# Kernel optimization log

Hardware: AMD Instinct MI355X
Metric: run time of the kernel (lower is better)

## Reference

```python
import jax, jax.numpy as jnp
import numpy as np

B, H, W, DIM = 2, 256, 256, 256
PDIM, HEADS = 128, 8
CH = PDIM // HEADS  # per-head channel dim (16)


def _dwconv3x3(x, w):
    # x: [b, c, h, w], w: [c, 1, 3, 3], depthwise (groups=c)
    return jax.lax.conv_general_dilated(
        x, w, window_strides=(1, 1), padding=((1, 1), (1, 1)),
        dimension_numbers=("NCHW", "OIHW", "NCHW"),
        feature_group_count=w.shape[0])


def setup_inputs() -> dict:
    key = jax.random.key(0)
    ks = jax.random.split(key, 8)

    def nrm(k, shape, fan):
        return jax.random.normal(k, shape, jnp.float32) / np.float32(np.sqrt(fan))

    x = jax.random.normal(ks[0], (B, H, W, DIM), jnp.float32)
    qkv_w = nrm(ks[1], (3 * PDIM, PDIM), PDIM)            # 1x1 conv, no bias
    dw_w = nrm(ks[2], (3 * PDIM, 1, 3, 3), 9)             # depthwise 3x3, no bias
    proj_w = nrm(ks[3], (DIM, DIM), DIM)                  # 1x1 conv, no bias
    g1_w = nrm(ks[4], (DIM // 2, DIM), DIM)               # gate conv1 (bias=True default)
    g1_b = jnp.zeros((DIM // 2,), jnp.float32)
    g2_w = nrm(ks[5], (1, DIM // 2), DIM // 2)            # gate conv2
    g2_b = jnp.zeros((1,), jnp.float32)
    temperature = jnp.ones((HEADS, 1, 1), jnp.float32)
    attn1 = jnp.array([0.2], jnp.float32)
    attn2 = jnp.array([0.2], jnp.float32)
    attn3 = jnp.array([0.2], jnp.float32)
    attn4 = jnp.array([0.2], jnp.float32)
    return dict(x=x, qkv_w=qkv_w, dw_w=dw_w, proj_w=proj_w, g1_w=g1_w,
                g1_b=g1_b, g2_w=g2_w, g2_b=g2_b, temperature=temperature,
                attn1=attn1, attn2=attn2, attn3=attn3, attn4=attn4)


def reference(x, qkv_w, dw_w, proj_w, g1_w, g1_b, g2_w, g2_b,
              temperature, attn1, attn2, attn3, attn4):
    xc = jnp.transpose(x, (0, 3, 1, 2))  # [b, dim, h, w]
    b, c, h, w = xc.shape
    x1, x2 = xc[:, :PDIM], xc[:, PDIM:]

    qkv = jnp.einsum('oc,bchw->bohw', qkv_w, x1)
    qkv = _dwconv3x3(qkv, dw_w)
    q, k, v = jnp.split(qkv, 3, axis=1)

    def to_heads(t):
        return t.reshape(b, HEADS, CH, h * w)  # [b, head, C, hw]

    q, k, v = to_heads(q), to_heads(k), to_heads(v)
    q = q / jnp.maximum(jnp.linalg.norm(q, axis=-1, keepdims=True), 1e-12)
    k = k / jnp.maximum(jnp.linalg.norm(k, axis=-1, keepdims=True), 1e-12)

    # gate -> scalar dynamic_k = int(C * mean(sigmoid(...)))
    g = jax.nn.relu(jnp.einsum('oc,bchw->bohw', g1_w, xc) + g1_b[None, :, None, None])
    g = jax.nn.sigmoid(jnp.einsum('oc,bchw->bohw', g2_w, g) + g2_b[None, :, None, None])
    dyn_k = jax.lax.stop_gradient(jnp.floor(CH * jnp.mean(g)))  # scalar float, grad-stopped like int()

    attn = jnp.einsum('bhcn,bhdn->bhcd', q, k) * temperature  # [b, head, C, C]
    # top-k mask via rank: rank[i,j] = position of attn[i,j] in descending sort of row i
    ranks = jnp.argsort(jnp.argsort(-attn, axis=-1), axis=-1)
    attn = jnp.where(ranks < dyn_k, attn, -jnp.inf)
    attn = jax.nn.softmax(attn, axis=-1)

    out_av = jnp.einsum('bhcd,bhdn->bhcn', attn, v)
    # out1..out4 are identical in the original; weighted sum collapses
    out = out_av * attn1 + out_av * attn2 + out_av * attn3 + out_av * attn4
    out = out.reshape(b, PDIM, h, w)
    out = jnp.einsum('oc,bchw->bohw', proj_w, jnp.concatenate([out, x2], axis=1))
    return jnp.transpose(out, (0, 2, 3, 1))  # [b, h, w, dim]
```

## Files before the change

kernel.cpp:

```cpp
#include <hip/hip_runtime.h>
#include <cstdint>
#include <cstddef>

typedef __attribute__((ext_vector_type(4))) float v4f;
typedef __attribute__((ext_vector_type(8))) short v8s;
typedef __attribute__((ext_vector_type(4))) short v4s;

__device__ __forceinline__ short f2bf(float f) {
  unsigned u = __float_as_uint(f);
  u += 0x7FFFu + ((u >> 16) & 1u);
  return (short)(u >> 16);
}
__device__ __forceinline__ float bf2f(short h) {
  return __uint_as_float(((unsigned)(unsigned short)h) << 16);
}
__device__ __forceinline__ v4f mfma16(v8s a, v8s b, v4f c) {
  return __builtin_amdgcn_mfma_f32_16x16x32_bf16(a, b, c, 0, 0, 0);
}

#define OFF_GRAM   0u
#define OFF_QN     32768u
#define OFF_KN     34816u
#define OFF_GSUM   36864u
#define OFF_ATTN   40960u
#define OFF_WQH    65536u
#define OFF_WQL    163840u
#define OFF_G1H    262144u
#define OFF_G1L    327680u
#define OFF_W2     393216u
#define OFF_QK     1048576u
#define OFF_V      135266304u
#define OFF_VOUT   168820736u

__global__ void k0_split(const float* __restrict__ qkv_w, const float* __restrict__ g1_w,
                         short* __restrict__ wqh, short* __restrict__ wql,
                         short* __restrict__ g1h, short* __restrict__ g1l) {
  const int t = blockIdx.x * 256 + threadIdx.x;
  if (t < 6144) {
    const int l = t & 63, ks = (t >> 6) & 3, g = t >> 8;
    const int n = g * 16 + (l & 15), k = ks * 32 + (l >> 4) * 8;
    v8s hi, lo;
#pragma unroll
    for (int j = 0; j < 8; ++j) {
      const float f = qkv_w[n * 128 + k + j];
      const short h = f2bf(f);
      hi[j] = h; lo[j] = f2bf(f - bf2f(h));
    }
    *(v8s*)(wqh + (size_t)t * 8) = hi;
    *(v8s*)(wql + (size_t)t * 8) = lo;
  } else if (t < 10240) {
    const int t2 = t - 6144;
    const int l = t2 & 63, ks2 = (t2 >> 6) & 7, g2 = t2 >> 9;
    const int n = g2 * 16 + (l & 15), k = ks2 * 32 + (l >> 4) * 8;
    v8s hi, lo;
#pragma unroll
    for (int j = 0; j < 8; ++j) {
      const float f = g1_w[n * 256 + k + j];
      const short h = f2bf(f);
      hi[j] = h; lo[j] = f2bf(f - bf2f(h));
    }
    *(v8s*)(g1h + (size_t)t2 * 8) = hi;
    *(v8s*)(g1l + (size_t)t2 * 8) = lo;
  }
}

__global__ __launch_bounds__(512, 4) void k1_qkv(const float* __restrict__ x,
                                                 const short* __restrict__ wqh,
                                                 const short* __restrict__ wql,
                                                 float* __restrict__ qkf,
                                                 short* __restrict__ vb) {
  __shared__ __align__(16) unsigned char sm[49152];
  const int tid = threadIdx.x;
  const size_t m0 = (size_t)blockIdx.x * 64;
  const int lane = tid & 63, wid = tid >> 6;
  const int wm = wid >> 2, wn = wid & 3;

  v8s pbh[3], pbl[3];
#pragma unroll
  for (int s = 0; s < 3; ++s) {
    const size_t off = ((size_t)((0 * 4 + wn) * 4 + s) * 64 + lane) * 8;
    pbh[s] = *(const v8s*)(wqh + off);
    pbl[s] = *(const v8s*)(wql + off);
  }

  {
    const int row = tid >> 3, c0 = (tid & 7) * 16;
    const float* src = x + (m0 + (size_t)row) * 256 + c0;
#pragma unroll
    for (int half = 0; half < 2; ++half) {
      v4f f0 = *(const v4f*)(src + half * 8);
      v4f f1 = *(const v4f*)(src + half * 8 + 4);
      v8s hi, lo;
#pragma unroll
      for (int j = 0; j < 4; ++j) {
        short h0 = f2bf(f0[j]); hi[j] = h0;   lo[j]   = f2bf(f0[j] - bf2f(h0));
        short h1 = f2bf(f1[j]); hi[4+j] = h1; lo[4+j] = f2bf(f1[j] - bf2f(h1));
      }
      const int col = c0 + half * 8;
      const int byo = (row * 256 + col * 2) ^ ((row & 7) << 4);
      *(v8s*)(sm + byo) = hi;
      *(v8s*)(sm + 16384 + byo) = lo;
    }
  }
  __syncthreads();
  v8s ah[4][2];
#pragma unroll
  for (int ks = 0; ks < 4; ++ks)
#pragma unroll
    for (int mi = 0; mi < 2; ++mi) {
      const int kb2 = (ks * 32 + ((lane >> 4) * 8)) * 2;
      const int m = wm * 32 + mi * 16 + (lane & 15);
      const int byoA = (m * 256 + kb2) ^ ((m & 7) << 4);
      ah[ks][mi] = *(const v8s*)(sm + byoA);
    }
  const v4f vz = {0.f, 0.f, 0.f, 0.f};
  v4f acc[6][2];
#pragma unroll
  for (int i = 0; i < 6; ++i) { acc[i][0] = vz; acc[i][1] = vz; }

#pragma unroll
  for (int s = 0; s < 24; ++s) {
    const int nc = s >> 2, ks = s & 3, slot = s % 3;
    const v8s bh = pbh[slot];
    const v8s bl = pbl[slot];
    if (s + 3 < 24) {
      const int s3 = s + 3, nc3 = s3 >> 2, ks3 = s3 & 3;
      const size_t off = ((size_t)((nc3 * 4 + wn) * 4 + ks3) * 64 + lane) * 8;
      pbh[slot] = *(const v8s*)(wqh + off);
      if (nc3 < 4) pbl[slot] = *(const v8s*)(wql + off);
    }
#pragma unroll
    for (int mi = 0; mi < 2; ++mi) {
      const int kb2 = (ks * 32 + ((lane >> 4) * 8)) * 2;
      const int m = wm * 32 + mi * 16 + (lane & 15);
      const int byoA = (m * 256 + kb2) ^ ((m & 7) << 4);
      acc[nc][mi] = mfma16(ah[ks][mi], bh, acc[nc][mi]);
      if (nc < 4) {
        const v8s alv = *(const v8s*)(sm + 16384 + byoA);
        acc[nc][mi] = mfma16(alv, bh, acc[nc][mi]);
        acc[nc][mi] = mfma16(ah[ks][mi], bl, acc[nc][mi]);
      }
    }
  }
#pragma unroll
  for (int nc = 0; nc < 4; ++nc)
#pragma unroll
    for (int mi = 0; mi < 2; ++mi)
#pragma unroll
      for (int r = 0; r < 4; ++r) {
        const int m = wm * 32 + mi * 16 + ((lane >> 4) * 4) + r;
        const int n = nc * 64 + wn * 16 + (lane & 15);
        qkf[(m0 + m) * 256 + n] = acc[nc][mi][r];
      }
  short* vtr = (short*)(sm + 32768);
#pragma unroll
  for (int nc = 4; nc < 6; ++nc)
#pragma unroll
    for (int mi = 0; mi < 2; ++mi)
#pragma unroll
      for (int r = 0; r < 4; ++r) {
        const int m = wm * 32 + mi * 16 + ((lane >> 4) * 4) + r;
        const int n = (nc - 4) * 64 + wn * 16 + (lane & 15);
        vtr[m * 128 + n] = f2bf(acc[nc][mi][r]);
      }
  __syncthreads();
  {
    const int base = tid * 8;
#pragma unroll
    for (int p = 0; p < 2; ++p) {
      const int flat = p * 4096 + base;
      const int row = flat >> 7, col = flat & 127;
      const v8s t = *(const v8s*)(vtr + row * 128 + col);
      *(v8s*)(vb + (m0 + row) * 128 + col) = t;
    }
  }
}

__global__ __launch_bounds__(512, 4) void k1_g(const float* __restrict__ x,
                                               const short* __restrict__ g1h,
                                               const short* __restrict__ g1l,
                                               const float* __restrict__ g1_b,
                                               const float* __restrict__ g2_w,
                                               const float* __restrict__ g2_b,
                                               double* __restrict__ gsum) {
  __shared__ __align__(16) unsigned char sm[32768];
  const int tid = threadIdx.x;
  const size_t m0 = (size_t)blockIdx.x * 64;
  const int lane = tid & 63, wid = tid >> 6;
  const int wm = wid >> 2, wn = wid & 3;
  const v4f vz = {0.f, 0.f, 0.f, 0.f};
  v4f acc[2][2];
  acc[0][0] = vz; acc[0][1] = vz; acc[1][0] = vz; acc[1][1] = vz;
  v8s pbh[3], pbl[3];
#pragma unroll
  for (int kc = 0; kc < 2; ++kc) {
#pragma unroll
    for (int s = 0; s < 3; ++s) {
      const int nc = s >> 2, ks = s & 3;
      const size_t off = ((size_t)((nc * 4 + wn) * 8 + kc * 4 + ks) * 64 + lane) * 8;
      pbh[s] = *(const v8s*)(g1h + off);
      pbl[s] = *(const v8s*)(g1l + off);
    }
    __syncthreads();
    {
      const int row = tid >> 3, c0 = (tid & 7) * 16;
      const float* src = x + (m0 + (size_t)row) * 256 + kc * 128 + c0;
#pragma unroll
      for (int half = 0; half < 2; ++half) {
        v4f f0 = *(const v4f*)(src + half * 8);
        v4f f1 = *(const v4f*)(src + half * 8 + 4);
        v8s hi, lo;
#pragma unroll
        for (int j = 0; j < 4; ++j) {
          short h0 = f2bf(f0[j]); hi[j] = h0;   lo[j]   = f2bf(f0[j] - bf2f(h0));
          short h1 = f2bf(f1[j]); hi[4+j] = h1; lo[4+j] = f2bf(f1[j] - bf2f(h1));
        }
        const int col = c0 + half * 8;
        const int byo = (row * 256 + col * 2) ^ ((row & 7) << 4);
        *(v8s*)(sm + byo) = hi;
        *(v8s*)(sm + 16384 + byo) = lo;
      }
    }
    __syncthreads();
    v8s ah[4][2];
#pragma unroll
    for (int ks = 0; ks < 4; ++ks)
#pragma unroll
      for (int mi = 0; mi < 2; ++mi) {
        const int kb2 = (ks * 32 + ((lane >> 4) * 8)) * 2;
        const int m = wm * 32 + mi * 16 + (lane & 15);
        const int byoA = (m * 256 + kb2) ^ ((m & 7) << 4);
        ah[ks][mi] = *(const v8s*)(sm + byoA);
      }
#pragma unroll
    for (int s = 0; s < 8; ++s) {
      const int nc = s >> 2, ks = s & 3, slot = s % 3;
      const v8s bh = pbh[slot];
      const v8s bl = pbl[slot];
      if (s + 3 < 8) {
        const int s3 = s + 3, nc3 = s3 >> 2, ks3 = s3 & 3;
        const size_t off = ((size_t)((nc3 * 4 + wn) * 8 + kc * 4 + ks3) * 64 + lane) * 8;
        pbh[slot] = *(const v8s*)(g1h + off);
        pbl[slot] = *(const v8s*)(g1l + off);
      }
#pragma unroll
      for (int mi = 0; mi < 2; ++mi) {
        const int kb2 = (ks * 32 + ((lane >> 4) * 8)) * 2;
        const int m = wm * 32 + mi * 16 + (lane & 15);
        const int byoA = (m * 256 + kb2) ^ ((m & 7) << 4);
        const v8s alv = *(const v8s*)(sm + 16384 + byoA);
        acc[nc][mi] = mfma16(ah[ks][mi], bh, acc[nc][mi]);
        acc[nc][mi] = mfma16(alv, bh, acc[nc][mi]);
        acc[nc][mi] = mfma16(ah[ks][mi], bl, acc[nc][mi]);
        acc[nc][mi] = mfma16(alv, bl, acc[nc][mi]);
      }
    }
  }
  __syncthreads();
  float* g2ws = (float*)sm;
  float* ldsg = (float*)(sm + 512);
  if (tid < 128) g2ws[tid] = g2_w[tid];
  if (tid < 64) ldsg[tid] = 0.f;
  __syncthreads();
  float bias[2], g2v[2];
#pragma unroll
  for (int nc = 0; nc < 2; ++nc) {
    const int n = nc * 64 + wn * 16 + (lane & 15);
    bias[nc] = g1_b[n];
    g2v[nc] = g2ws[n];
  }
#pragma unroll
  for (int mi = 0; mi < 2; ++mi)
#pragma unroll
    for (int r = 0; r < 4; ++r) {
      float part = 0.f;
#pragma unroll
      for (int nc = 0; nc < 2; ++nc) {
        float val = acc[nc][mi][r] + bias[nc];
        val = fmaxf(val, 0.f);
        part += val * g2v[nc];
      }
      part += __shfl_xor(part, 1, 16);
      part += __shfl_xor(part, 2, 16);
      part += __shfl_xor(part, 4, 16);
      part += __shfl_xor(part, 8, 16);
      if ((lane & 15) == 0)
        atomicAdd(&ldsg[wm * 32 + mi * 16 + ((lane >> 4) * 4) + r], part);
    }
  __syncthreads();
  if (tid < 64) {
    float pre = ldsg[tid] + g2_b[0];
    float g = 1.f / (1.f + expf(-pre));
#pragma unroll
    for (int mk = 1; mk < 64; mk <<= 1) g += __shfl_xor(g, mk, 64);
    if (tid == 0) atomicAdd(gsum, (double)g);
  }
}

__global__ __launch_bounds__(256, 4) void k2_conv(const float* __restrict__ qkf,
                                                  const short* __restrict__ vb,
                                                  const float* __restrict__ dw_w,
                                                  double* __restrict__ gram,
                                                  double* __restrict__ qn,
                                                  double* __restrict__ kn,
                                                  short* __restrict__ vbuf) {
  __shared__ __align__(16) unsigned char SM[25984];
  float* haloT = (float*)SM;
  short* vtr   = (short*)SM;
  float* wsm   = (float*)(SM + 20800);
  float* redQ  = (float*)(SM + 21376);
  float* redK  = (float*)(SM + 21632);
  float* gramW = (float*)(SM + 21888);

  const int tid = threadIdx.x;
  const int tile = blockIdx.x, h = blockIdx.y, b = blockIdx.z;
  const int px0 = (tile & 15) * 16, py0 = (tile >> 4) * 16;
  const int c = tid & 15, r = tid >> 4;
  const int lane = tid & 63, w4 = tid >> 6;

  auto stage = [&](int sec) {
    const int chbase = sec * 128 + h * 16;
#pragma unroll
    for (int i = 0; i < 6; ++i) {
      const int idx = tid + i * 256;
      if (idx < 1296) {
        const int p = idx >> 2, e4 = (idx & 3) * 4;
        const int row = p / 18, col = p - row * 18;
        const int gy = py0 - 1 + row, gx = px0 - 1 + col;
        v4f val = {0.f, 0.f, 0.f, 0.f};
        if (gy >= 0 && gy < 256 && gx >= 0 && gx < 256) {
          const size_t pix = (size_t)(b * 65536 + gy * 256 + gx);
          if (sec < 2) {
            val = *(const v4f*)(qkf + pix * 256 + sec * 128 + h * 16 + e4);
          } else {
            const v4s sv = *(const v4s*)(vb + pix * 128 + h * 16 + e4);
            val[0] = bf2f(sv[0]); val[1] = bf2f(sv[1]);
            val[2] = bf2f(sv[2]); val[3] = bf2f(sv[3]);
          }
        }
        haloT[(e4 + 0) * 325 + p] = val[0];
        haloT[(e4 + 1) * 325 + p] = val[1];
        haloT[(e4 + 2) * 325 + p] = val[2];
        haloT[(e4 + 3) * 325 + p] = val[3];
      }
    }
    if (tid < 144) wsm[tid] = dw_w[chbase * 9 + tid];
  };

  auto conv16 = [&](float* o) {
#pragma unroll
    for (int j = 0; j < 16; ++j) o[j] = 0.f;
#pragma unroll
    for (int dy = 0; dy < 3; ++dy) {
      const float* rp = haloT + c * 325 + (r + dy) * 18;
      float rowb[18];
#pragma unroll
      for (int xx = 0; xx < 18; ++xx) rowb[xx] = rp[xx];
      const float w0 = wsm[c * 9 + dy * 3 + 0];
      const float w1 = wsm[c * 9 + dy * 3 + 1];
      const float w2 = wsm[c * 9 + dy * 3 + 2];
#pragma unroll
      for (int j = 0; j < 16; ++j)
        o[j] += w0 * rowb[j] + w1 * rowb[j + 1] + w2 * rowb[j + 2];
    }
  };

  float qreg[16], kreg[16];

  stage(0);
  __syncthreads();
  conv16(qreg);
  {
    float s = 0.f;
#pragma unroll
    for (int j = 0; j < 16; ++j) s += qreg[j] * qreg[j];
    s += __shfl_xor(s, 16, 64);
    s += __shfl_xor(s, 32, 64);
    if (lane < 16) redQ[w4 * 16 + lane] = s;
  }
  __syncthreads();
  stage(1);
  __syncthreads();
  conv16(kreg);
  {
    float s = 0.f;
#pragma unroll
    for (int j = 0; j < 16; ++j) s += kreg[j] * kreg[j];
    s += __shfl_xor(s, 16, 64);
    s += __shfl_xor(s, 32, 64);
    if (lane < 16) redK[w4 * 16 + lane] = s;
  }
  {
    v4f acc = {0.f, 0.f, 0.f, 0.f};
    const int qt = lane >> 4;
    const bool hiHalf = (qt & 1);
#pragma unroll
    for (int f = 0; f < 2; ++f) {
      const int src = ((f * 2 + (qt >> 1)) << 4) | (lane & 15);
      v8s qh, ql, kh, kl;
#pragma unroll
      for (int j = 0; j < 8; ++j) {
        const float qa = __shfl(qreg[j], src, 64);
        const float qb = __shfl(qreg[j + 8], src, 64);
        const float ka = __shfl(kreg[j], src, 64);
        const float kb = __shfl(kreg[j + 8], src, 64);
        const float qv = hiHalf ? qb : qa;
        const float kv = hiHalf ? kb : ka;
        const short h1 = f2bf(qv); qh[j] = h1; ql[j] = f2bf(qv - bf2f(h1));
        const short h2 = f2bf(kv); kh[j] = h2; kl[j] = f2bf(kv - bf2f(h2));
      }
      acc = mfma16(qh, kh, acc);
      acc = mfma16(ql, kh, acc);
      acc = mfma16(qh, kl, acc);
      acc = mfma16(ql, kl, acc);
    }
#pragma unroll
    for (int rr = 0; rr < 4; ++rr)
      gramW[w4 * 256 + (qt * 4 + rr) * 16 + (lane & 15)] = acc[rr];
  }
  __syncthreads();
  stage(2);
  __syncthreads();
  float vv[16];
  conv16(vv);
  if (tid < 16) {
    const float t = redQ[tid] + redQ[16 + tid] + redQ[32 + tid] + redQ[48 + tid];
    atomicAdd(&qn[b * 128 + h * 16 + tid], (double)t);
  } else if (tid < 32) {
    const int cc = tid - 16;
    const float t = redK[cc] + redK[16 + cc] + redK[32 + cc] + redK[48 + cc];
    atomicAdd(&kn[b * 128 + h * 16 + cc], (double)t);
  }
  {
    const float g = gramW[tid] + gramW[256 + tid] + gramW[512 + tid] + gramW[768 + tid];
    atomicAdd(&gram[(size_t)(b * 8 + h) * 256 + tid], (double)g);
  }
  __syncthreads();
  {
#pragma unroll
    for (int j = 0; j < 16; ++j) vtr[(r * 16 + j) * 24 + c] = f2bf(vv[j]);
  }
  __syncthreads();
  {
    const v8s o0 = *(const v8s*)(vtr + tid * 24);
    const v8s o1 = *(const v8s*)(vtr + tid * 24 + 8);
    short* dst = vbuf + ((size_t)b * 65536 + (size_t)(py0 + (tid >> 4)) * 256 + (px0 + (tid & 15))) * 128 + h * 16;
    *(v8s*)dst = o0;
    *(v8s*)(dst + 8) = o1;
  }
}

__global__ void k3a_attn(const double* __restrict__ gram, const double* __restrict__ qn,
                         const double* __restrict__ kn, const double* __restrict__ gsum,
                         const float* __restrict__ temp,
                         const float* __restrict__ a1p, const float* __restrict__ a2p,
                         const float* __restrict__ a3p, const float* __restrict__ a4p,
                         float* __restrict__ attnw) {
  const int t = threadIdx.x;
  const int b = t >> 7, rem = t & 127, h = rem >> 4, c = rem & 15;
  const float qnv = fmaxf(sqrtf((float)qn[b * 128 + h * 16 + c]), 1e-12f);
  const float tv = temp[h];
  float a[16];
#pragma unroll
  for (int d = 0; d < 16; ++d) {
    const float knv = fmaxf(sqrtf((float)kn[b * 128 + h * 16 + d]), 1e-12f);
    a[d] = (float)gram[(size_t)(b * 8 + h) * 256 + c * 16 + d] / (qnv * knv) * tv;
  }
  const float dynk = floorf(16.f * (float)(gsum[0] / 131072.0));
  float mx = -INFINITY;
  bool keep[16];
#pragma unroll
  for (int d = 0; d < 16; ++d) {
    int rank = 0;
#pragma unroll
    for (int e = 0; e < 16; ++e)
      rank += ((a[e] > a[d]) || ((a[e] == a[d]) && (e < d))) ? 1 : 0;
    keep[d] = ((float)rank < dynk);
    if (keep[d]) mx = fmaxf(mx, a[d]);
  }
  float ssum = 0.f, wvv[16];
#pragma unroll
  for (int d = 0; d < 16; ++d) {
    wvv[d] = keep[d] ? expf(a[d] - mx) : 0.f;
    ssum += wvv[d];
  }
  const float satt = a1p[0] + a2p[0] + a3p[0] + a4p[0];
  const float sc = satt / ssum;
#pragma unroll
  for (int d = 0; d < 16; ++d) attnw[t * 16 + d] = wvv[d] * sc;
}

__global__ void k3b_fold(const float* __restrict__ proj_w, const float* __restrict__ attnw,
                         short* __restrict__ W2f) {
  const int g = blockIdx.x, b = blockIdx.y;
  const int ks = threadIdx.x >> 6, lane = threadIdx.x & 63;
  const int o = g * 16 + (lane & 15);
  const int k0 = ks * 32 + (lane >> 4) * 8;
  v8s outv;
  if (k0 < 128) {
    const int h = k0 >> 4, d0 = k0 & 15;
    float s[8];
#pragma unroll
    for (int j = 0; j < 8; ++j) s[j] = 0.f;
#pragma unroll
    for (int i = 0; i < 16; ++i) {
      const float pw = proj_w[o * 256 + h * 16 + i];
#pragma unroll
      for (int j = 0; j < 8; ++j)
        s[j] += pw * attnw[((b * 8 + h) * 16 + i) * 16 + d0 + j];
    }
#pragma unroll
    for (int j = 0; j < 8; ++j) outv[j] = f2bf(s[j]);
  } else {
#pragma unroll
    for (int j = 0; j < 8; ++j) outv[j] = f2bf(proj_w[o * 256 + k0 + j]);
  }
  *(v8s*)(W2f + ((size_t)(b * 128 + g * 8 + ks) * 64 + lane) * 8) = outv;
}

__global__ __launch_bounds__(512, 4) void k4_out(const short* __restrict__ vbuf,
                                                 const float* __restrict__ x,
                                                 const short* __restrict__ W2f,
                                                 float* __restrict__ out) {
  __shared__ __align__(16) unsigned char sm[32768];
  const int tid = threadIdx.x;
  const size_t m0 = (size_t)blockIdx.x * 64;
  const int b = (int)(m0 >> 16);
  const int lane = tid & 63, wid = tid >> 6;
  const int wm = wid >> 2, wn = wid & 3;

  v8s pbB[3];
#pragma unroll
  for (int s = 0; s < 3; ++s) {
    const size_t off = ((size_t)(b * 128 + (0 * 4 + wn) * 8 + s) * 64 + lane) * 8;
    pbB[s] = *(const v8s*)(W2f + off);
  }
  {
    const int row = tid >> 3, c0 = (tid & 7) * 16;
    {
      const short* src = vbuf + (m0 + (size_t)row) * 128 + c0;
#pragma unroll
      for (int half = 0; half < 2; ++half) {
        const int col = c0 + half * 8;
        const int byo = (row * 512 + col * 2) ^ ((row & 7) << 4);
        *(v8s*)(sm + byo) = *(const v8s*)(src + half * 8);
      }
    }
    {
      const float* src = x + (m0 + (size_t)row) * 256 + 128 + c0;
#pragma unroll
      for (int half = 0; half < 2; ++half) {
        v4f f0 = *(const v4f*)(src + half * 8);
        v4f f1 = *(const v4f*)(src + half * 8 + 4);
        v8s hv;
#pragma unroll
        for (int j = 0; j < 4; ++j) { hv[j] = f2bf(f0[j]); hv[4+j] = f2bf(f1[j]); }
        const int col = 128 + c0 + half * 8;
        const int byo = (row * 512 + col * 2) ^ ((row & 7) << 4);
        *(v8s*)(sm + byo) = hv;
      }
    }
  }
  __syncthreads();
  v8s af[8][2];
#pragma unroll
  for (int ks = 0; ks < 8; ++ks)
#pragma unroll
    for (int mi = 0; mi < 2; ++mi) {
      const int kb2 = (ks * 32 + ((lane >> 4) * 8)) * 2;
      const int m = wm * 32 + mi * 16 + (lane & 15);
      const int byoA = (m * 512 + kb2) ^ ((m & 7) << 4);
      af[ks][mi] = *(const v8s*)(sm + byoA);
    }
  const v4f vz = {0.f, 0.f, 0.f, 0.f};
  v4f acc[4][2];
#pragma unroll
  for (int i = 0; i < 4; ++i) { acc[i][0] = vz; acc[i][1] = vz; }
#pragma unroll
  for (int s = 0; s < 32; ++s) {
    const int nc = s >> 3, ks = s & 7, slot = s % 3;
    const v8s bf = pbB[slot];
    if (s + 3 < 32) {
      const int s3 = s + 3, nc3 = s3 >> 3, ks3 = s3 & 7;
      const size_t off = ((size_t)(b * 128 + (nc3 * 4 + wn) * 8 + ks3) * 64 + lane) * 8;
      pbB[slot] = *(const v8s*)(W2f + off);
    }
#pragma unroll
    for (int mi = 0; mi < 2; ++mi)
      acc[nc][mi] = mfma16(af[ks][mi], bf, acc[nc][mi]);
  }
#pragma unroll
  for (int nc = 0; nc < 4; ++nc)
#pragma unroll
    for (int mi = 0; mi < 2; ++mi)
#pragma unroll
      for (int r = 0; r < 4; ++r) {
        const int m = wm * 32 + mi * 16 + ((lane >> 4) * 4) + r;
        const int o = nc * 64 + wn * 16 + (lane & 15);
        out[(m0 + m) * 256 + o] = acc[nc][mi][r];
      }
}

extern "C" void kernel_launch(void* const* d_in, const int* in_sizes, int n_in,
                              void* d_out, int out_size, void* d_ws, size_t ws_size,
                              hipStream_t stream) {
  const float* x      = (const float*)d_in[0];
  const float* qkv_w  = (const float*)d_in[1];
  const float* dw_w   = (const float*)d_in[2];
  const float* proj_w = (const float*)d_in[3];
  const float* g1_w   = (const float*)d_in[4];
  const float* g1_b   = (const float*)d_in[5];
  const float* g2_w   = (const float*)d_in[6];
  const float* g2_b   = (const float*)d_in[7];
  const float* temp   = (const float*)d_in[8];
  const float* a1     = (const float*)d_in[9];
  const float* a2     = (const float*)d_in[10];
  const float* a3     = (const float*)d_in[11];
  const float* a4     = (const float*)d_in[12];
  float* out = (float*)d_out;
  char* ws = (char*)d_ws;

  double* gram  = (double*)(ws + OFF_GRAM);
  double* qn    = (double*)(ws + OFF_QN);
  double* kn    = (double*)(ws + OFF_KN);
  double* gsum  = (double*)(ws + OFF_GSUM);
  float*  attnw = (float*)(ws + OFF_ATTN);
  short*  wqh   = (short*)(ws + OFF_WQH);
  short*  wql   = (short*)(ws + OFF_WQL);
  short*  g1h   = (short*)(ws + OFF_G1H);
  short*  g1l   = (short*)(ws + OFF_G1L);
  short*  W2f   = (short*)(ws + OFF_W2);
  float*  qkf   = (float*)(ws + OFF_QK);
  short*  vb    = (short*)(ws + OFF_V);
  short*  vbuf  = (short*)(ws + OFF_VOUT);

  hipMemsetAsync(ws, 0, 40960, stream);
  k0_split<<<40, 256, 0, stream>>>(qkv_w, g1_w, wqh, wql, g1h, g1l);
  k1_qkv<<<2048, 512, 0, stream>>>(x, wqh, wql, qkf, vb);
  k1_g<<<2048, 512, 0, stream>>>(x, g1h, g1l, g1_b, g2_w, g2_b, gsum);
  k2_conv<<<dim3(256, 8, 2), 256, 0, stream>>>(qkf, vb, dw_w, gram, qn, kn, vbuf);
  k3a_attn<<<1, 256, 0, stream>>>(gram, qn, kn, gsum, temp, a1, a2, a3, a4, attnw);
  k3b_fold<<<dim3(16, 2), 512, 0, stream>>>(proj_w, attnw, W2f);
  k4_out<<<2048, 512, 0, stream>>>(vbuf, x, W2f, out);
  (void)in_sizes; (void)n_in; (void)out_size; (void)ws_size;
}
```

Before: 291.8 us.

## Prefetch conv halo stages into registers, pad LDS rows, use packed bf16 splits

The depthwise conv kernel now loads the next section's halo from global memory into registers while computing the current convolution, then writes it to LDS after the barrier. This overlaps global latency with compute. The halo layout is padded to 20-float rows so each conv row can be read with vector LDS loads. Across kernels, the hi/lo bf16 split switches to truncation for the hi part plus a packed round-to-nearest conversion for the lo part, cutting per-element conversion ALU work. The trade-off is higher register pressure from the prefetch buffers and slightly larger LDS use, which may lower occupancy under launch_bounds(256,4).

```diff
diff --git a/kernel.cpp b/kernel.cpp
--- a/kernel.cpp
+++ b/kernel.cpp
@@ -1,10 +1,12 @@
 #include <hip/hip_runtime.h>
+#include <hip/hip_bf16.h>
 #include <cstdint>
 #include <cstddef>
 
 typedef __attribute__((ext_vector_type(4))) float v4f;
 typedef __attribute__((ext_vector_type(8))) short v8s;
 typedef __attribute__((ext_vector_type(4))) short v4s;
+typedef __attribute__((ext_vector_type(4))) unsigned v4u;
 
 __device__ __forceinline__ short f2bf(float f) {
   unsigned u = __float_as_uint(f);
@@ -16,6 +18,21 @@
 }
 __device__ __forceinline__ v4f mfma16(v8s a, v8s b, v4f c) {
   return __builtin_amdgcn_mfma_f32_16x16x32_bf16(a, b, c, 0, 0, 0);
+}
+__device__ __forceinline__ unsigned pack_rn(float a, float b) {
+  __hip_bfloat162 p = __float22bfloat162_rn(make_float2(a, b));
+  union { __hip_bfloat162 v; unsigned u; } c; c.v = p; return c.u;
+}
+struct u2 { unsigned h, l; };
+__device__ __forceinline__ u2 split2pk(float a, float b) {
+  const unsigned ua = __float_as_uint(a) & 0xffff0000u;
+  const unsigned ub = __float_as_uint(b) & 0xffff0000u;
+  const float la = a - __uint_as_float(ua);
+  const float lb = b - __uint_as_float(ub);
+  u2 r;
+  r.h = (ua >> 16) | ub;
+  r.l = pack_rn(la, lb);
+  return r;
 }
 
 #define OFF_GRAM   0u
@@ -90,16 +107,15 @@
     for (int half = 0; half < 2; ++half) {
       v4f f0 = *(const v4f*)(src + half * 8);
       v4f f1 = *(const v4f*)(src + half * 8 + 4);
-      v8s hi, lo;
-#pragma unroll
-      for (int j = 0; j < 4; ++j) {
-        short h0 = f2bf(f0[j]); hi[j] = h0;   lo[j]   = f2bf(f0[j] - bf2f(h0));
-        short h1 = f2bf(f1[j]); hi[4+j] = h1; lo[4+j] = f2bf(f1[j] - bf2f(h1));
-      }
+      v4u hi, lo;
+      u2 t0 = split2pk(f0[0], f0[1]); hi[0] = t0.h; lo[0] = t0.l;
+      u2 t1 = split2pk(f0[2], f0[3]); hi[1] = t1.h; lo[1] = t1.l;
+      u2 t2 = split2pk(f1[0], f1[1]); hi[2] = t2.h; lo[2] = t2.l;
+      u2 t3 = split2pk(f1[2], f1[3]); hi[3] = t3.h; lo[3] = t3.l;
       const int col = c0 + half * 8;
       const int byo = (row * 256 + col * 2) ^ ((row & 7) << 4);
-      *(v8s*)(sm + byo) = hi;
-      *(v8s*)(sm + 16384 + byo) = lo;
+      *(v4u*)(sm + byo) = hi;
+      *(v4u*)(sm + 16384 + byo) = lo;
     }
   }
   __syncthreads();
@@ -209,16 +225,15 @@
       for (int half = 0; half < 2; ++half) {
         v4f f0 = *(const v4f*)(src + half * 8);
         v4f f1 = *(const v4f*)(src + half * 8 + 4);
-        v8s hi, lo;
-#pragma unroll
-        for (int j = 0; j < 4; ++j) {
-          short h0 = f2bf(f0[j]); hi[j] = h0;   lo[j]   = f2bf(f0[j] - bf2f(h0));
-          short h1 = f2bf(f1[j]); hi[4+j] = h1; lo[4+j] = f2bf(f1[j] - bf2f(h1));
-        }
+        v4u hi, lo;
+        u2 t0 = split2pk(f0[0], f0[1]); hi[0] = t0.h; lo[0] = t0.l;
+        u2 t1 = split2pk(f0[2], f0[3]); hi[1] = t1.h; lo[1] = t1.l;
+        u2 t2 = split2pk(f1[0], f1[1]); hi[2] = t2.h; lo[2] = t2.l;
+        u2 t3 = split2pk(f1[2], f1[3]); hi[3] = t3.h; lo[3] = t3.l;
         const int col = c0 + half * 8;
         const int byo = (row * 256 + col * 2) ^ ((row & 7) << 4);
-        *(v8s*)(sm + byo) = hi;
-        *(v8s*)(sm + 16384 + byo) = lo;
+        *(v4u*)(sm + byo) = hi;
+        *(v4u*)(sm + 16384 + byo) = lo;
       }
     }
     __syncthreads();
@@ -304,13 +319,13 @@
                                                   double* __restrict__ qn,
                                                   double* __restrict__ kn,
                                                   short* __restrict__ vbuf) {
-  __shared__ __align__(16) unsigned char SM[25984];
+  __shared__ __align__(16) unsigned char SM[28480];
   float* haloT = (float*)SM;
   short* vtr   = (short*)SM;
-  float* wsm   = (float*)(SM + 20800);
-  float* redQ  = (float*)(SM + 21376);
-  float* redK  = (float*)(SM + 21632);
-  float* gramW = (float*)(SM + 21888);
+  float* wsm   = (float*)(SM + 23296);
+  float* redQ  = (float*)(SM + 23872);
+  float* redK  = (float*)(SM + 24128);
+  float* gramW = (float*)(SM + 24384);
 
   const int tid = threadIdx.x;
   const int tile = blockIdx.x, h = blockIdx.y, b = blockIdx.z;
@@ -318,16 +333,16 @@
   const int c = tid & 15, r = tid >> 4;
   const int lane = tid & 63, w4 = tid >> 6;
 
-  auto stage = [&](int sec) {
+  auto stage_load = [&](int sec, v4f* vals) {
     const int chbase = sec * 128 + h * 16;
 #pragma unroll
     for (int i = 0; i < 6; ++i) {
       const int idx = tid + i * 256;
+      v4f val = {0.f, 0.f, 0.f, 0.f};
       if (idx < 1296) {
         const int p = idx >> 2, e4 = (idx & 3) * 4;
         const int row = p / 18, col = p - row * 18;
         const int gy = py0 - 1 + row, gx = px0 - 1 + col;
-        v4f val = {0.f, 0.f, 0.f, 0.f};
         if (gy >= 0 && gy < 256 && gx >= 0 && gx < 256) {
           const size_t pix = (size_t)(b * 65536 + gy * 256 + gx);
           if (sec < 2) {
@@ -338,37 +353,57 @@
             val[2] = bf2f(sv[2]); val[3] = bf2f(sv[3]);
           }
         }
-        haloT[(e4 + 0) * 325 + p] = val[0];
-        haloT[(e4 + 1) * 325 + p] = val[1];
-        haloT[(e4 + 2) * 325 + p] = val[2];
-        haloT[(e4 + 3) * 325 + p] = val[3];
-      }
-    }
-    if (tid < 144) wsm[tid] = dw_w[chbase * 9 + tid];
+      }
+      vals[i] = val;
+    }
   };
+  auto stage_write = [&](int sec, const v4f* vals) {
+#pragma unroll
+    for (int i = 0; i < 6; ++i) {
+      const int idx = tid + i * 256;
+      if (idx < 1296) {
+        const int p = idx >> 2, e4 = (idx & 3) * 4;
+        const int row = p / 18, col = p - row * 18;
+        haloT[(e4 + 0) * 364 + row * 20 + col] = vals[i][0];
+        haloT[(e4 + 1) * 364 + row * 20 + col] = vals[i][1];
+        haloT[(e4 + 2) * 364 + row * 20 + col] = vals[i][2];
+        haloT[(e4 + 3) * 364 + row * 20 + col] = vals[i][3];
+      }
+    }
+    if (tid < 144) wsm[tid] = dw_w[(sec * 128 + h * 16) * 9 + tid];
+  };
 
   auto conv16 = [&](float* o) {
 #pragma unroll
     for (int j = 0; j < 16; ++j) o[j] = 0.f;
 #pragma unroll
     for (int dy = 0; dy < 3; ++dy) {
-      const float* rp = haloT + c * 325 + (r + dy) * 18;
-      float rowb[18];
-#pragma unroll
-      for (int xx = 0; xx < 18; ++xx) rowb[xx] = rp[xx];
+      const float* rp = haloT + c * 364 + (r + dy) * 20;
+      const v4f t0 = *(const v4f*)(rp);
+      const v4f t1 = *(const v4f*)(rp + 4);
+      const v4f t2 = *(const v4f*)(rp + 8);
+      const v4f t3 = *(const v4f*)(rp + 12);
+      float rb[18];
+#pragma unroll
+      for (int q = 0; q < 4; ++q) { rb[q] = t0[q]; rb[4+q] = t1[q]; rb[8+q] = t2[q]; rb[12+q] = t3[q]; }
+      rb[16] = rp[16]; rb[17] = rp[17];
       const float w0 = wsm[c * 9 + dy * 3 + 0];
       const float w1 = wsm[c * 9 + dy * 3 + 1];
       const float w2 = wsm[c * 9 + dy * 3 + 2];
 #pragma unroll
       for (int j = 0; j < 16; ++j)
-        o[j] += w0 * rowb[j] + w1 * rowb[j + 1] + w2 * rowb[j + 2];
+        o[j] += w0 * rb[j] + w1 * rb[j + 1] + w2 * rb[j + 2];
     }
   };
 
   float qreg[16], kreg[16];
-
-  stage(0);
-  __syncthreads();
+  v4f sbuf[6];
+
+  stage_load(0, sbuf);
+  stage_write(0, sbuf);
+  __syncthreads();
+  v4f sk[6];
+  stage_load(1, sk);
   conv16(qreg);
   {
     float s = 0.f;
@@ -379,8 +414,10 @@
     if (lane < 16) redQ[w4 * 16 + lane] = s;
   }
   __syncthreads();
-  stage(1);
-  __syncthreads();
+  stage_write(1, sk);
+  __syncthreads();
+  v4f sv[6];
+  stage_load(2, sv);
   conv16(kreg);
   {
     float s = 0.f;
@@ -397,18 +434,26 @@
 #pragma unroll
     for (int f = 0; f < 2; ++f) {
       const int src = ((f * 2 + (qt >> 1)) << 4) | (lane & 15);
-      v8s qh, ql, kh, kl;
-#pragma unroll
-      for (int j = 0; j < 8; ++j) {
-        const float qa = __shfl(qreg[j], src, 64);
-        const float qb = __shfl(qreg[j + 8], src, 64);
-        const float ka = __shfl(kreg[j], src, 64);
-        const float kb = __shfl(kreg[j + 8], src, 64);
-        const float qv = hiHalf ? qb : qa;
-        const float kv = hiHalf ? kb : ka;
-        const short h1 = f2bf(qv); qh[j] = h1; ql[j] = f2bf(qv - bf2f(h1));
-        const short h2 = f2bf(kv); kh[j] = h2; kl[j] = f2bf(kv - bf2f(h2));
-      }
+      v4u qh4, ql4, kh4, kl4;
+#pragma unroll
+      for (int jj = 0; jj < 4; ++jj) {
+        const float q0a = __shfl(qreg[2 * jj], src, 64);
+        const float q0b = __shfl(qreg[2 * jj + 8], src, 64);
+        const float q1a = __shfl(qreg[2 * jj + 1], src, 64);
+        const float q1b = __shfl(qreg[2 * jj + 9], src, 64);
+        const float k0a = __shfl(kreg[2 * jj], src, 64);
+        const float k0b = __shfl(kreg[2 * jj + 8], src, 64);
+        const float k1a = __shfl(kreg[2 * jj + 1], src, 64);
+        const float k1b = __shfl(kreg[2 * jj + 9], src, 64);
+        const float q0 = hiHalf ? q0b : q0a, q1 = hiHalf ? q1b : q1a;
+        const float k0 = hiHalf ? k0b : k0a, k1 = hiHalf ? k1b : k1a;
+        const u2 tq = split2pk(q0, q1); qh4[jj] = tq.h; ql4[jj] = tq.l;
+        const u2 tk = split2pk(k0, k1); kh4[jj] = tk.h; kl4[jj] = tk.l;
+      }
+      const v8s qh = __builtin_bit_cast(v8s, qh4);
+      const v8s ql = __builtin_bit_cast(v8s, ql4);
+      const v8s kh = __builtin_bit_cast(v8s, kh4);
+      const v8s kl = __builtin_bit_cast(v8s, kl4);
       acc = mfma16(qh, kh, acc);
       acc = mfma16(ql, kh, acc);
       acc = mfma16(qh, kl, acc);
@@ -419,7 +464,7 @@
       gramW[w4 * 256 + (qt * 4 + rr) * 16 + (lane & 15)] = acc[rr];
   }
   __syncthreads();
-  stage(2);
+  stage_write(2, sv);
   __syncthreads();
   float vv[16];
   conv16(vv);
@@ -552,12 +597,12 @@
       for (int half = 0; half < 2; ++half) {
         v4f f0 = *(const v4f*)(src + half * 8);
         v4f f1 = *(const v4f*)(src + half * 8 + 4);
-        v8s hv;
-#pragma unroll
-        for (int j = 0; j < 4; ++j) { hv[j] = f2bf(f0[j]); hv[4+j] = f2bf(f1[j]); }
+        v4u hv;
+        hv[0] = pack_rn(f0[0], f0[1]); hv[1] = pack_rn(f0[2], f0[3]);
+        hv[2] = pack_rn(f1[0], f1[1]); hv[3] = pack_rn(f1[2], f1[3]);
         const int col = 128 + c0 + half * 8;
         const int byo = (row * 512 + col * 2) ^ ((row & 7) << 4);
-        *(v8s*)(sm + byo) = hv;
+        *(v4u*)(sm + byo) = hv;
       }
     }
   }
```

After: 280.1 us. 4.0% less time.
